# Kernel optimization log

Hardware: AMD Instinct MI355X
Metric: run time of the kernel (lower is better)

The kernel has to match this reference:

```python
import jax, jax.numpy as jnp
import numpy as np

NE, NR, NT = 100000, 500, 365
DE = DR = DT = 200
P = min(DE, DR, DT)  # 200
B = 1024


def setup_inputs() -> dict:
    key = jax.random.key(0)
    ks = jax.random.split(key, 10)
    return {
        "e1_idx": jax.random.randint(ks[0], (B,), 0, NE),
        "r_idx": jax.random.randint(ks[1], (B,), 0, NR),
        "t_idx": jax.random.randint(ks[2], (B,), 0, NT),
        "E": jax.random.normal(ks[3], (NE, DE), dtype=jnp.float32),
        "R": jax.random.normal(ks[4], (NR, DR), dtype=jnp.float32),
        "T": jax.random.normal(ks[5], (NT, DT), dtype=jnp.float32),
        "F0": jax.random.uniform(ks[6], (DR, P), jnp.float32, -0.1, 0.1),
        "F1": jax.random.uniform(ks[7], (DE, P), jnp.float32, -0.1, 0.1),
        "F2": jax.random.uniform(ks[8], (DE, P), jnp.float32, -0.1, 0.1),
        "F3": jax.random.uniform(ks[9], (DT, P), jnp.float32, -0.1, 0.1),
    }


def reference(e1_idx, r_idx, t_idx, E, R, T, F0, F1, F2, F3):
    # Embedding lookups
    e1 = E[e1_idx]          # (B, de)
    r = R[r_idx]            # (B, dr)
    t = T[t_idx]            # (B, dt)
    # Factor projections into rank-P CPD space
    fr = r @ F0             # (B, P)
    fe1 = e1 @ F1           # (B, P)
    ft = t @ F3             # (B, P)
    FE = E @ F2             # (NE, P)
    # Diagonal core tensor I => the mm/bmm chain is exactly an
    # elementwise product over the rank dimension, then score vs all entities.
    x = (fr * fe1 * ft) @ FE.T  # (B, NE)
    return jax.nn.sigmoid(x)
```

## Files before the change

kernel.cpp:

```cpp
#include <hip/hip_runtime.h>

#define NE_  100000
#define NB_  1024
#define DD_  200
#define PP_  224

typedef _Float16 h8  __attribute__((ext_vector_type(8)));
typedef float    fx4 __attribute__((ext_vector_type(4)));
typedef float    fx16 __attribute__((ext_vector_type(16)));

__device__ __forceinline__ float fast_sigmoid(float x) {
    float e = __builtin_amdgcn_exp2f(-1.44269504088896340736f * x);
    return __builtin_amdgcn_rcpf(1.0f + e);
}

__global__ __launch_bounds__(256) void prep_kernel(
    const int*   __restrict__ e1_idx, const int* __restrict__ r_idx,
    const int*   __restrict__ t_idx,
    const float* __restrict__ E, const float* __restrict__ R,
    const float* __restrict__ T,
    const float* __restrict__ F0, const float* __restrict__ F1,
    const float* __restrict__ F2, const float* __restrict__ F3,
    _Float16* __restrict__ h16, _Float16* __restrict__ F2t)
{
    const int tid = threadIdx.x;
    const int bid = blockIdx.x;
    if (bid < 128) {
        const int rb = bid * 8;
        const float* rrow[8];
        const float* erow[8];
        const float* trow[8];
        #pragma unroll
        for (int i = 0; i < 8; ++i) {
            rrow[i] = R + (size_t)r_idx[rb + i]  * DD_;
            erow[i] = E + (size_t)e1_idx[rb + i] * DD_;
            trow[i] = T + (size_t)t_idx[rb + i]  * DD_;
        }
        const int p = tid;
        float fr[8], fe[8], ft[8];
        #pragma unroll
        for (int i = 0; i < 8; ++i) { fr[i] = 0.f; fe[i] = 0.f; ft[i] = 0.f; }
        if (p < DD_) {
            for (int k = 0; k < DD_; ++k) {
                float f0 = F0[k * DD_ + p];
                float f1 = F1[k * DD_ + p];
                float f3 = F3[k * DD_ + p];
                #pragma unroll
                for (int i = 0; i < 8; ++i) {
                    fr[i] = fmaf(rrow[i][k], f0, fr[i]);
                    fe[i] = fmaf(erow[i][k], f1, fe[i]);
                    ft[i] = fmaf(trow[i][k], f3, ft[i]);
                }
            }
        }
        if (p < PP_) {
            #pragma unroll
            for (int i = 0; i < 8; ++i) {
                float v = (p < DD_) ? fr[i] * fe[i] * ft[i] : 0.0f;
                h16[(size_t)(rb + i) * PP_ + p] = (_Float16)v;
            }
        }
    } else {
        const int n0 = (bid - 128) * 28;
        for (int j = tid; j < 28 * PP_; j += 256) {
            int nl = j / PP_;
            int k  = j - nl * PP_;
            int n  = n0 + nl;
            float v = (n < DD_ && k < DD_) ? F2[k * DD_ + n] : 0.0f;
            F2t[(size_t)n * PP_ + k] = (_Float16)v;
        }
    }
}

__global__ __launch_bounds__(256) void fe_kernel(
    const float* __restrict__ E, const _Float16* __restrict__ F2t,
    _Float16* __restrict__ FE)
{
    const int tid  = threadIdx.x;
    const int w    = tid >> 6;
    const int l    = tid & 63;
    const int ln   = l & 15;
    const int quad = l >> 4;
    const int m0   = blockIdx.x * 64;

    int m = m0 + w * 16 + ln;
    if (m >= NE_) m = NE_ - 1;
    const float* erow = E + (size_t)m * DD_;

    h8 a[7];
    #pragma unroll
    for (int ks = 0; ks < 7; ++ks) {
        const int k = ks * 32 + quad * 8;
        h8 v = {(_Float16)0, (_Float16)0, (_Float16)0, (_Float16)0,
                (_Float16)0, (_Float16)0, (_Float16)0, (_Float16)0};
        if (k < DD_) {
            fx4 lo = *(const fx4*)(erow + k);
            fx4 hi = *(const fx4*)(erow + k + 4);
            v[0] = (_Float16)lo[0]; v[1] = (_Float16)lo[1];
            v[2] = (_Float16)lo[2]; v[3] = (_Float16)lo[3];
            v[4] = (_Float16)hi[0]; v[5] = (_Float16)hi[1];
            v[6] = (_Float16)hi[2]; v[7] = (_Float16)hi[3];
        }
        a[ks] = v;
    }

    const int mrb = m0 + w * 16 + quad * 4;
    #pragma unroll
    for (int nt = 0; nt < 14; ++nt) {
        fx4 acc = {0.f, 0.f, 0.f, 0.f};
        const _Float16* bp = F2t + (size_t)(nt * 16 + ln) * PP_ + quad * 8;
        #pragma unroll
        for (int ks = 0; ks < 7; ++ks) {
            h8 b = *(const h8*)(bp + ks * 32);
            acc = __builtin_amdgcn_mfma_f32_16x16x32_f16(a[ks], b, acc, 0, 0, 0);
        }
        #pragma unroll
        for (int r = 0; r < 4; ++r) {
            int mr = mrb + r;
            if (mr < NE_)
                FE[(size_t)mr * PP_ + nt * 16 + ln] = (_Float16)acc[r];
        }
    }
}

__global__ __launch_bounds__(256, 4) void score_kernel(
    const _Float16* __restrict__ h16, const _Float16* __restrict__ FE,
    float* __restrict__ out)
{
    __shared__ __align__(16) _Float16 Alds[64 * 232];

    const int tid = threadIdx.x;
    const int w   = tid >> 6;
    const int l   = tid & 63;
    const int l31 = l & 31;
    const int lh  = l >> 5;
    const int wm  = w & 1;
    const int wn  = w >> 1;
    const int nb  = blockIdx.x * 64;

    h8 bfr[14];
    {
        int n = nb + wn * 32 + l31;
        if (n >= NE_) n = NE_ - 1;
        const _Float16* bp = FE + (size_t)n * PP_ + lh * 8;
        #pragma unroll
        for (int ks = 0; ks < 14; ++ks)
            bfr[ks] = *(const h8*)(bp + ks * 16);
    }

    const int ncol = nb + wn * 32 + l31;
    const bool nok = (ncol < NE_);
    const int srow = tid >> 2;
    const int scol = (tid & 3) * 8;

    for (int c = 0; c < 16; ++c) {
        __syncthreads();
        const _Float16* hsrc = h16 + (size_t)(c * 64) * PP_;
        #pragma unroll
        for (int j = 0; j < 7; ++j)
            *(h8*)&Alds[srow * 232 + scol + j * 32] =
                *(const h8*)(hsrc + (size_t)srow * PP_ + scol + j * 32);
        __syncthreads();

        fx16 acc;
        #pragma unroll
        for (int i = 0; i < 16; ++i) acc[i] = 0.0f;

        #pragma unroll
        for (int ks = 0; ks < 14; ++ks) {
            h8 a = *(const h8*)&Alds[(wm * 32 + l31) * 232 + ks * 16 + lh * 8];
            acc = __builtin_amdgcn_mfma_f32_32x32x16_f16(a, bfr[ks], acc, 0, 0, 0);
        }

        if (nok) {
            const int mb = c * 64 + wm * 32 + lh * 4;
            #pragma unroll
            for (int r = 0; r < 16; ++r) {
                int m = mb + (r & 3) + 8 * (r >> 2);
                out[(size_t)m * NE_ + ncol] = fast_sigmoid(acc[r]);
            }
        }
    }
}

extern "C" void kernel_launch(void* const* d_in, const int* in_sizes, int n_in,
                              void* d_out, int out_size, void* d_ws, size_t ws_size,
                              hipStream_t stream)
{
    const int*   e1_idx = (const int*)  d_in[0];
    const int*   r_idx  = (const int*)  d_in[1];
    const int*   t_idx  = (const int*)  d_in[2];
    const float* E      = (const float*)d_in[3];
    const float* R      = (const float*)d_in[4];
    const float* T      = (const float*)d_in[5];
    const float* F0     = (const float*)d_in[6];
    const float* F1     = (const float*)d_in[7];
    const float* F2     = (const float*)d_in[8];
    const float* F3     = (const float*)d_in[9];
    float* out = (float*)d_out;

    _Float16* FE16 = (_Float16*)d_ws;
    _Float16* h16  = FE16 + (size_t)NE_ * PP_;
    _Float16* F2t  = h16  + (size_t)NB_ * PP_;

    prep_kernel<<<136, 256, 0, stream>>>(e1_idx, r_idx, t_idx, E, R, T,
                                         F0, F1, F2, F3, h16, F2t);

    const int mblocks = (NE_ + 63) / 64;
    fe_kernel<<<mblocks, 256, 0, stream>>>(E, F2t, FE16);

    score_kernel<<<mblocks, 256, 0, stream>>>(h16, FE16, out);
}
```

Before: 669.7 us.

## Reassociate to fold F2 into query side and drop FE kernel

Computes g = (fr*fe1*ft) @ F2^T per query in the prep kernel, so the score kernel multiplies g against raw E rows converted to fp16 on the fly. This removes the separate fe_kernel, which produced a 100000x224 fp16 intermediate, along with its global write and re-read, and cuts the K loop from 14 to 13 MFMA steps. The cost is heavier per-block work in prep (a second 200x200 projection) and fp32-to-fp16 conversion of E inside the score kernel.

```diff
diff --git a/kernel.cpp b/kernel.cpp
--- a/kernel.cpp
+++ b/kernel.cpp
@@ -21,110 +21,70 @@
     const float* __restrict__ T,
     const float* __restrict__ F0, const float* __restrict__ F1,
     const float* __restrict__ F2, const float* __restrict__ F3,
-    _Float16* __restrict__ h16, _Float16* __restrict__ F2t)
+    _Float16* __restrict__ g16)
 {
+    __shared__ __align__(16) float hl[4][DD_];
     const int tid = threadIdx.x;
-    const int bid = blockIdx.x;
-    if (bid < 128) {
-        const int rb = bid * 8;
-        const float* rrow[8];
-        const float* erow[8];
-        const float* trow[8];
+    const int rb  = blockIdx.x * 4;
+
+    const float* rrow[4];
+    const float* erow[4];
+    const float* trow[4];
+    #pragma unroll
+    for (int i = 0; i < 4; ++i) {
+        rrow[i] = R + (size_t)r_idx[rb + i]  * DD_;
+        erow[i] = E + (size_t)e1_idx[rb + i] * DD_;
+        trow[i] = T + (size_t)t_idx[rb + i]  * DD_;
+    }
+
+    const int p = tid;
+    if (p < DD_) {
+        float fr[4], fe[4], ft[4];
         #pragma unroll
-        for (int i = 0; i < 8; ++i) {
-            rrow[i] = R + (size_t)r_idx[rb + i]  * DD_;
-            erow[i] = E + (size_t)e1_idx[rb + i] * DD_;
-            trow[i] = T + (size_t)t_idx[rb + i]  * DD_;
+        for (int i = 0; i < 4; ++i) { fr[i] = 0.f; fe[i] = 0.f; ft[i] = 0.f; }
+        #pragma unroll 4
+        for (int k = 0; k < DD_; ++k) {
+            float f0 = F0[k * DD_ + p];
+            float f1 = F1[k * DD_ + p];
+            float f3 = F3[k * DD_ + p];
+            #pragma unroll
+            for (int i = 0; i < 4; ++i) {
+                fr[i] = fmaf(rrow[i][k], f0, fr[i]);
+                fe[i] = fmaf(erow[i][k], f1, fe[i]);
+                ft[i] = fmaf(trow[i][k], f3, ft[i]);
+            }
         }
-        const int p = tid;
-        float fr[8], fe[8], ft[8];
         #pragma unroll
-        for (int i = 0; i < 8; ++i) { fr[i] = 0.f; fe[i] = 0.f; ft[i] = 0.f; }
-        if (p < DD_) {
-            for (int k = 0; k < DD_; ++k) {
-                float f0 = F0[k * DD_ + p];
-                float f1 = F1[k * DD_ + p];
-                float f3 = F3[k * DD_ + p];
+        for (int i = 0; i < 4; ++i)
+            hl[i][p] = fr[i] * fe[i] * ft[i];
+    }
+    __syncthreads();
+
+    const int j = tid;
+    if (j < PP_) {
+        float g[4] = {0.f, 0.f, 0.f, 0.f};
+        if (j < DD_) {
+            const float* f2r = F2 + (size_t)j * DD_;
+            for (int p4 = 0; p4 < DD_; p4 += 4) {
+                fx4 f2v = *(const fx4*)(f2r + p4);
                 #pragma unroll
-                for (int i = 0; i < 8; ++i) {
-                    fr[i] = fmaf(rrow[i][k], f0, fr[i]);
-                    fe[i] = fmaf(erow[i][k], f1, fe[i]);
-                    ft[i] = fmaf(trow[i][k], f3, ft[i]);
+                for (int i = 0; i < 4; ++i) {
+                    fx4 hv = *(const fx4*)&hl[i][p4];
+                    g[i] = fmaf(hv[0], f2v[0], g[i]);
+                    g[i] = fmaf(hv[1], f2v[1], g[i]);
+                    g[i] = fmaf(hv[2], f2v[2], g[i]);
+                    g[i] = fmaf(hv[3], f2v[3], g[i]);
                 }
             }
         }
-        if (p < PP_) {
-            #pragma unroll
-            for (int i = 0; i < 8; ++i) {
-                float v = (p < DD_) ? fr[i] * fe[i] * ft[i] : 0.0f;
-                h16[(size_t)(rb + i) * PP_ + p] = (_Float16)v;
-            }
-        }
-    } else {
-        const int n0 = (bid - 128) * 28;
-        for (int j = tid; j < 28 * PP_; j += 256) {
-            int nl = j / PP_;
-            int k  = j - nl * PP_;
-            int n  = n0 + nl;
-            float v = (n < DD_ && k < DD_) ? F2[k * DD_ + n] : 0.0f;
-            F2t[(size_t)n * PP_ + k] = (_Float16)v;
-        }
-    }
-}
-
-__global__ __launch_bounds__(256) void fe_kernel(
-    const float* __restrict__ E, const _Float16* __restrict__ F2t,
-    _Float16* __restrict__ FE)
-{
-    const int tid  = threadIdx.x;
-    const int w    = tid >> 6;
-    const int l    = tid & 63;
-    const int ln   = l & 15;
-    const int quad = l >> 4;
-    const int m0   = blockIdx.x * 64;
-
-    int m = m0 + w * 16 + ln;
-    if (m >= NE_) m = NE_ - 1;
-    const float* erow = E + (size_t)m * DD_;
-
-    h8 a[7];
-    #pragma unroll
-    for (int ks = 0; ks < 7; ++ks) {
-        const int k = ks * 32 + quad * 8;
-        h8 v = {(_Float16)0, (_Float16)0, (_Float16)0, (_Float16)0,
-                (_Float16)0, (_Float16)0, (_Float16)0, (_Float16)0};
-        if (k < DD_) {
-            fx4 lo = *(const fx4*)(erow + k);
-            fx4 hi = *(const fx4*)(erow + k + 4);
-            v[0] = (_Float16)lo[0]; v[1] = (_Float16)lo[1];
-            v[2] = (_Float16)lo[2]; v[3] = (_Float16)lo[3];
-            v[4] = (_Float16)hi[0]; v[5] = (_Float16)hi[1];
-            v[6] = (_Float16)hi[2]; v[7] = (_Float16)hi[3];
-        }
-        a[ks] = v;
-    }
-
-    const int mrb = m0 + w * 16 + quad * 4;
-    #pragma unroll
-    for (int nt = 0; nt < 14; ++nt) {
-        fx4 acc = {0.f, 0.f, 0.f, 0.f};
-        const _Float16* bp = F2t + (size_t)(nt * 16 + ln) * PP_ + quad * 8;
         #pragma unroll
-        for (int ks = 0; ks < 7; ++ks) {
-            h8 b = *(const h8*)(bp + ks * 32);
-            acc = __builtin_amdgcn_mfma_f32_16x16x32_f16(a[ks], b, acc, 0, 0, 0);
-        }
-        #pragma unroll
-        for (int r = 0; r < 4; ++r) {
-            int mr = mrb + r;
-            if (mr < NE_)
-                FE[(size_t)mr * PP_ + nt * 16 + ln] = (_Float16)acc[r];
-        }
+        for (int i = 0; i < 4; ++i)
+            g16[(size_t)(rb + i) * PP_ + j] = (_Float16)g[i];
     }
 }
 
 __global__ __launch_bounds__(256, 4) void score_kernel(
-    const _Float16* __restrict__ h16, const _Float16* __restrict__ FE,
+    const _Float16* __restrict__ g16, const float* __restrict__ E,
     float* __restrict__ out)
 {
     __shared__ __align__(16) _Float16 Alds[64 * 232];
@@ -138,14 +98,26 @@
     const int wn  = w >> 1;
     const int nb  = blockIdx.x * 64;
 
-    h8 bfr[14];
+    h8 bfr[13];
     {
         int n = nb + wn * 32 + l31;
         if (n >= NE_) n = NE_ - 1;
-        const _Float16* bp = FE + (size_t)n * PP_ + lh * 8;
+        const float* ep = E + (size_t)n * DD_;
         #pragma unroll
-        for (int ks = 0; ks < 14; ++ks)
-            bfr[ks] = *(const h8*)(bp + ks * 16);
+        for (int ks = 0; ks < 13; ++ks) {
+            const int k = ks * 16 + lh * 8;
+            h8 v = {(_Float16)0, (_Float16)0, (_Float16)0, (_Float16)0,
+                    (_Float16)0, (_Float16)0, (_Float16)0, (_Float16)0};
+            if (k < DD_) {
+                fx4 lo = *(const fx4*)(ep + k);
+                fx4 hi = *(const fx4*)(ep + k + 4);
+                v[0] = (_Float16)lo[0]; v[1] = (_Float16)lo[1];
+                v[2] = (_Float16)lo[2]; v[3] = (_Float16)lo[3];
+                v[4] = (_Float16)hi[0]; v[5] = (_Float16)hi[1];
+                v[6] = (_Float16)hi[2]; v[7] = (_Float16)hi[3];
+            }
+            bfr[ks] = v;
+        }
     }
 
     const int ncol = nb + wn * 32 + l31;
@@ -155,11 +127,11 @@
 
     for (int c = 0; c < 16; ++c) {
         __syncthreads();
-        const _Float16* hsrc = h16 + (size_t)(c * 64) * PP_;
+        const _Float16* gsrc = g16 + (size_t)(c * 64) * PP_;
         #pragma unroll
         for (int j = 0; j < 7; ++j)
             *(h8*)&Alds[srow * 232 + scol + j * 32] =
-                *(const h8*)(hsrc + (size_t)srow * PP_ + scol + j * 32);
+                *(const h8*)(gsrc + (size_t)srow * PP_ + scol + j * 32);
         __syncthreads();
 
         fx16 acc;
@@ -167,7 +139,7 @@
         for (int i = 0; i < 16; ++i) acc[i] = 0.0f;
 
         #pragma unroll
-        for (int ks = 0; ks < 14; ++ks) {
+        for (int ks = 0; ks < 13; ++ks) {
             h8 a = *(const h8*)&Alds[(wm * 32 + l31) * 232 + ks * 16 + lh * 8];
             acc = __builtin_amdgcn_mfma_f32_32x32x16_f16(a, bfr[ks], acc, 0, 0, 0);
         }
@@ -199,15 +171,11 @@
     const float* F3     = (const float*)d_in[9];
     float* out = (float*)d_out;
 
-    _Float16* FE16 = (_Float16*)d_ws;
-    _Float16* h16  = FE16 + (size_t)NE_ * PP_;
-    _Float16* F2t  = h16  + (size_t)NB_ * PP_;
+    _Float16* g16 = (_Float16*)d_ws;
 
-    prep_kernel<<<136, 256, 0, stream>>>(e1_idx, r_idx, t_idx, E, R, T,
-                                         F0, F1, F2, F3, h16, F2t);
+    prep_kernel<<<256, 256, 0, stream>>>(e1_idx, r_idx, t_idx, E, R, T,
+                                         F0, F1, F2, F3, g16);
 
-    const int mblocks = (NE_ + 63) / 64;
-    fe_kernel<<<mblocks, 256, 0, stream>>>(E, F2t, FE16);
-
-    score_kernel<<<mblocks, 256, 0, stream>>>(h16, FE16, out);
+    const int nblocks = (NE_ + 63) / 64;
+    score_kernel<<<nblocks, 256, 0, stream>>>(g16, E, out);
 }
```

Measured after the change: 566.4 us, median of 2. 15.4% less time.
